# Performance work log

Hardware: AMD Instinct MI355X
Metric: run time of the kernel (lower is better)

The kernel has to match this reference:

```python
import jax, jax.numpy as jnp
import numpy as np

B = 131072
_CNOT_PERM = np.array([0, 1, 3, 2])  # |c t>: 10<->11 swap


def _apply_1q(psi, mats, wire):
    # psi: [B,2,2,2,2] complex, mats: [B,2,2] complex, per-sample single-qubit gate on `wire`
    psi = jnp.moveaxis(psi, wire + 1, -1)
    sh = psi.shape
    psi = psi.reshape(sh[0], -1, 2)
    psi = jnp.einsum('bij,bkj->bki', mats, psi)
    return jnp.moveaxis(psi.reshape(sh), -1, wire + 1)


def _cnot_adj(psi, w):
    # CNOT with control=w, target=w+1 (adjacent wires)
    psi = jnp.moveaxis(psi, (w + 1, w + 2), (-2, -1))
    sh = psi.shape
    psi = psi.reshape(sh[:-2] + (4,))[..., _CNOT_PERM].reshape(sh)
    return jnp.moveaxis(psi, (-2, -1), (w + 1, w + 2))


def _circuit(enc):
    # enc: [B,4] rotation angles; returns [B,4] PauliZ expectations
    b = enc.shape[0]
    half = 0.5 * enc
    c = jnp.cos(half).astype(jnp.complex64)
    s = jnp.sin(half).astype(jnp.complex64)
    z = jnp.zeros_like(c)
    ph = jnp.exp(-1j * half.astype(jnp.complex64))
    ry = jnp.stack([jnp.stack([c, -s], -1), jnp.stack([s, c], -1)], -2)   # [B,4,2,2]
    rz = jnp.stack([jnp.stack([ph, z], -1), jnp.stack([z, jnp.conj(ph)], -1)], -2)
    rx = jnp.stack([jnp.stack([c, -1j * s], -1), jnp.stack([-1j * s, c], -1)], -2)
    psi = jnp.zeros((b, 2, 2, 2, 2), jnp.complex64).at[:, 0, 0, 0, 0].set(1.0)
    for w in range(4):
        psi = _apply_1q(psi, ry[:, w], w)
    for w in range(4):
        psi = _apply_1q(psi, rz[:, w], w)
    for w in range(3):
        psi = _cnot_adj(psi, w)
    for w in range(4):
        psi = _apply_1q(psi, rx[:, w], w)
    probs = psi.real ** 2 + psi.imag ** 2  # [B,2,2,2,2]
    expz = []
    for w in range(4):
        p = jnp.moveaxis(probs, w + 1, 1).reshape(b, 2, -1).sum(-1)
        expz.append(p[:, 0] - p[:, 1])
    return jnp.stack(expz, -1)  # [B,4]


def setup_inputs() -> dict:
    key = jax.random.key(0)
    ks = jax.random.split(key, 9)
    f32 = jnp.float32
    return {
        'x': jax.random.normal(ks[0], (B, 1, 24, 24), f32),
        'W_enc': jax.random.normal(ks[1], (4, 16), f32) * 0.25,
        'b_enc': jax.random.normal(ks[2], (4,), f32) * 0.25,
        'W1': jax.random.normal(ks[3], (32, 4), f32) * 0.5,
        'b1': jax.random.normal(ks[4], (32,), f32) * 0.5,
        'W2': jax.random.normal(ks[5], (4, 32), f32) * 0.17,
        'b2': jax.random.normal(ks[6], (4,), f32) * 0.17,
        'gamma': jnp.ones((4,), f32),
        'beta': jnp.zeros((4,), f32),
    }


def reference(x, W_enc, b_enc, W1, b1, W2, b2, gamma, beta):
    bsz = x.shape[0]
    # avg_pool2d(x, 6): 24x24 -> 4x4, then flatten to 16
    pooled = x.reshape(bsz, 1, 4, 6, 4, 6).mean((3, 5)).reshape(bsz, 16)
    encoded = pooled @ W_enc.T + b_enc            # [B,4]
    out_q = _circuit(encoded)                      # [B,4]
    h = jax.nn.relu(out_q @ W1.T + b1)             # [B,32]
    out = h @ W2.T + b2                            # [B,num_classes]
    # BatchNorm1d in training mode (biased batch variance, eps=1e-5)
    mean = out.mean(0)
    var = ((out - mean) ** 2).mean(0)
    return gamma * (out - mean) / jnp.sqrt(var + 1e-5) + beta
```

## Files before the change

### kernel.cpp

```cpp
#include <hip/hip_runtime.h>

#define BATCH      131072
#define NBLK_MAIN  512
#define NBLK_BN    512

__global__ __launch_bounds__(256, 2) void qnat_main(
    const float* __restrict__ x,
    const float* __restrict__ Wenc, const float* __restrict__ benc,
    const float* __restrict__ W1,   const float* __restrict__ b1,
    const float* __restrict__ W2,   const float* __restrict__ b2,
    float* __restrict__ out_pre, float* __restrict__ partials)
{
    __shared__ float sW[360];
    __shared__ __align__(16) float stage[4][2320];
    __shared__ float pbuf[4][1088];
    __shared__ float redS[4][8];

    const int t = threadIdx.x;
    if (t < 64)  sW[t]       = Wenc[t];
    if (t < 4)   sW[64 + t]  = benc[t];
    if (t < 128) sW[68 + t]  = W1[t];
    if (t < 32)  sW[196 + t] = b1[t];
    if (t < 128) sW[228 + t] = W2[t];
    if (t < 4)   sW[356 + t] = b2[t];
    __syncthreads();

    const int wave = t >> 6, lane = t & 63;
    const int sampleBase = blockIdx.x * 256 + wave * 64;
    float* st = stage[wave];
    float* pb = pbuf[wave];

    const int s_loc = lane >> 4;
    const int slot  = lane & 15;
    const int spr   = slot >> 2, spc = slot & 3;
    const int rdOff = s_loc * 580 + spr * 144 + spc * 6;

    const float4* xg = reinterpret_cast<const float4*>(x);
    const unsigned gbase = (unsigned)sampleBase * 144u;

    float pv[16];
    #pragma unroll
    for (int c = 0; c < 16; ++c) {
        float4 v[9];
        #pragma unroll
        for (int i = 0; i < 9; ++i)
            v[i] = xg[gbase + (unsigned)c * 576u + (unsigned)i * 64u + (unsigned)lane];
        #pragma unroll
        for (int i = 0; i < 9; ++i) {
            const int g = i * 64 + lane;
            const int s = g / 144;
            const int q = g - s * 144;
            *reinterpret_cast<float4*>(&st[s * 580 + q * 4]) = v[i];
        }
        float acc = 0.f;
        #pragma unroll
        for (int r = 0; r < 6; ++r) {
            const float2 a  = *reinterpret_cast<const float2*>(&st[rdOff + r * 24 + 0]);
            const float2 bb = *reinterpret_cast<const float2*>(&st[rdOff + r * 24 + 2]);
            const float2 cc = *reinterpret_cast<const float2*>(&st[rdOff + r * 24 + 4]);
            acc += a.x + a.y + bb.x + bb.y + cc.x + cc.y;
        }
        pv[c] = acc * (1.f / 36.f);
    }

    #pragma unroll
    for (int c = 0; c < 16; ++c)
        pb[(c * 4 + s_loc) * 17 + slot] = pv[c];
    float pooled[16];
    #pragma unroll
    for (int q = 0; q < 16; ++q)
        pooled[q] = pb[lane * 17 + q];

    float ch[4], sh[4];
    #pragma unroll
    for (int j = 0; j < 4; ++j) {
        float e = sW[64 + j];
        #pragma unroll
        for (int k = 0; k < 16; ++k) e = fmaf(pooled[k], sW[j * 16 + k], e);
        const float h = 0.5f * e;
        ch[j] = cosf(h);
        sh[j] = sinf(h);
    }

    float re[16], im[16];
    #pragma unroll
    for (int i = 0; i < 16; ++i) { re[i] = 0.f; im[i] = 0.f; }
    re[0] = 1.f;

    #pragma unroll
    for (int w = 0; w < 4; ++w) {
        const int bit = 8 >> w;
        #pragma unroll
        for (int i = 0; i < 16; ++i) if (!(i & bit)) {
            const int jj = i | bit;
            const float r0 = re[i], m0 = im[i], r1 = re[jj], m1 = im[jj];
            re[i]  = ch[w] * r0 - sh[w] * r1;  im[i]  = ch[w] * m0 - sh[w] * m1;
            re[jj] = sh[w] * r0 + ch[w] * r1;  im[jj] = sh[w] * m0 + ch[w] * m1;
        }
    }
    #pragma unroll
    for (int w = 0; w < 4; ++w) {
        const int bit = 8 >> w;
        #pragma unroll
        for (int i = 0; i < 16; ++i) {
            const float sg = (i & bit) ? 1.f : -1.f;
            const float r = re[i], m = im[i];
            re[i] = ch[w] * r - sg * sh[w] * m;
            im[i] = ch[w] * m + sg * sh[w] * r;
        }
    }
    #define SWAP_AMP(a, b) { float tr = re[a]; re[a] = re[b]; re[b] = tr; \
                             float ti = im[a]; im[a] = im[b]; im[b] = ti; }
    SWAP_AMP(8, 12)  SWAP_AMP(9, 13)  SWAP_AMP(10, 14) SWAP_AMP(11, 15)
    SWAP_AMP(4, 6)   SWAP_AMP(5, 7)   SWAP_AMP(12, 14) SWAP_AMP(13, 15)
    SWAP_AMP(2, 3)   SWAP_AMP(6, 7)   SWAP_AMP(10, 11) SWAP_AMP(14, 15)
    #undef SWAP_AMP

    #pragma unroll
    for (int w = 0; w < 4; ++w) {
        const int bit = 8 >> w;
        #pragma unroll
        for (int i = 0; i < 16; ++i) if (!(i & bit)) {
            const int jj = i | bit;
            const float r0 = re[i], m0 = im[i], r1 = re[jj], m1 = im[jj];
            re[i]  = ch[w] * r0 + sh[w] * m1;  im[i]  = ch[w] * m0 - sh[w] * r1;
            re[jj] = sh[w] * m0 + ch[w] * r1;  im[jj] = ch[w] * m1 - sh[w] * r0;
        }
    }

    float ez[4];
    #pragma unroll
    for (int w = 0; w < 4; ++w) {
        const int bit = 8 >> w;
        float acc = 0.f;
        #pragma unroll
        for (int i = 0; i < 16; ++i) {
            const float p = re[i] * re[i] + im[i] * im[i];
            acc += (i & bit) ? -p : p;
        }
        ez[w] = acc;
    }

    float o0 = sW[356], o1 = sW[357], o2 = sW[358], o3 = sW[359];
    #pragma unroll
    for (int i = 0; i < 32; ++i) {
        float h = sW[196 + i];
        #pragma unroll
        for (int j = 0; j < 4; ++j) h = fmaf(ez[j], sW[68 + i * 4 + j], h);
        h = fmaxf(h, 0.f);
        o0 = fmaf(h, sW[228 +  0 + i], o0);
        o1 = fmaf(h, sW[228 + 32 + i], o1);
        o2 = fmaf(h, sW[228 + 64 + i], o2);
        o3 = fmaf(h, sW[228 + 96 + i], o3);
    }

    reinterpret_cast<float4*>(out_pre)[blockIdx.x * 256 + t] =
        make_float4(o0, o1, o2, o3);

    {
        float v8[8] = { o0, o1, o2, o3, o0 * o0, o1 * o1, o2 * o2, o3 * o3 };
        #pragma unroll
        for (int off = 32; off; off >>= 1) {
            #pragma unroll
            for (int k = 0; k < 8; ++k) v8[k] += __shfl_down(v8[k], off);
        }
        if (lane == 0) {
            #pragma unroll
            for (int k = 0; k < 8; ++k) redS[wave][k] = v8[k];
        }
        __syncthreads();
        if (t < 8) {
            partials[blockIdx.x * 8 + t] =
                redS[0][t] + redS[1][t] + redS[2][t] + redS[3][t];
        }
    }
}

__global__ __launch_bounds__(512) void qnat_reduce(
    const float* __restrict__ partials, const float* __restrict__ gamma,
    const float* __restrict__ beta, float* __restrict__ ss)
{
    const int t = threadIdx.x;
    const float4* p4 = reinterpret_cast<const float4*>(partials);
    const float4 a = p4[t * 2], b = p4[t * 2 + 1];
    float v[8] = { a.x, a.y, a.z, a.w, b.x, b.y, b.z, b.w };
    #pragma unroll
    for (int off = 32; off; off >>= 1) {
        #pragma unroll
        for (int k = 0; k < 8; ++k) v[k] += __shfl_down(v[k], off);
    }
    __shared__ float red[8][8];
    const int wave = t >> 6, lane = t & 63;
    if (lane == 0) {
        #pragma unroll
        for (int k = 0; k < 8; ++k) red[wave][k] = v[k];
    }
    __syncthreads();
    if (t < 4) {
        float sum = 0.f, sumsq = 0.f;
        #pragma unroll
        for (int w = 0; w < 8; ++w) { sum += red[w][t]; sumsq += red[w][4 + t]; }
        const float invB  = 1.f / (float)BATCH;
        const float mean  = sum * invB;
        const float var   = sumsq * invB - mean * mean;
        const float scale = gamma[t] / sqrtf(var + 1e-5f);
        ss[t]     = scale;
        ss[4 + t] = beta[t] - mean * scale;
    }
}

__global__ __launch_bounds__(256) void qnat_bn(
    float* __restrict__ io, const float* __restrict__ ss)
{
    __shared__ float s8[8];
    if (threadIdx.x < 8) s8[threadIdx.x] = ss[threadIdx.x];
    __syncthreads();
    const int idx = blockIdx.x * 256 + threadIdx.x;
    float4* p = reinterpret_cast<float4*>(io);
    float4 v = p[idx];
    v.x = fmaf(v.x, s8[0], s8[4]);
    v.y = fmaf(v.y, s8[1], s8[5]);
    v.z = fmaf(v.z, s8[2], s8[6]);
    v.w = fmaf(v.w, s8[3], s8[7]);
    p[idx] = v;
}

extern "C" void kernel_launch(void* const* d_in, const int* in_sizes, int n_in,
                              void* d_out, int out_size, void* d_ws, size_t ws_size,
                              hipStream_t stream)
{
    const float* x     = (const float*)d_in[0];
    const float* Wenc  = (const float*)d_in[1];
    const float* benc  = (const float*)d_in[2];
    const float* W1    = (const float*)d_in[3];
    const float* b1    = (const float*)d_in[4];
    const float* W2    = (const float*)d_in[5];
    const float* b2    = (const float*)d_in[6];
    const float* gamma = (const float*)d_in[7];
    const float* beta  = (const float*)d_in[8];

    float* out      = (float*)d_out;
    float* partials = (float*)d_ws;
    float* ss       = partials + NBLK_MAIN * 8;

    qnat_main<<<NBLK_MAIN, 256, 0, stream>>>(x, Wenc, benc, W1, b1, W2, b2,
                                             out, partials);
    qnat_reduce<<<1, 512, 0, stream>>>(partials, gamma, beta, ss);
    qnat_bn<<<NBLK_BN, 256, 0, stream>>>(out, ss);
}
```

Baseline: 59.77 us.

## Split each sample across two lanes and double the main-kernel grid

The main kernel now processes 32 samples per wave instead of 64, with two lanes sharing each sample. Each lane computes half of the encoder dot product and the halves are combined with a shuffle. The separate pooling buffer is dropped and the staging buffer reused, which lowers LDS use so the launch bound can ask for 4 blocks per CU. The grid doubles to 1024 blocks and the reduce kernel sums twice as many partials. The cost is that both lanes of a pair run the full quantum-circuit and MLP math redundantly, and the new block-wide __syncthreads calls add barriers.

```diff
diff --git a/kernel.cpp b/kernel.cpp
--- a/kernel.cpp
+++ b/kernel.cpp
@@ -1,10 +1,10 @@
 #include <hip/hip_runtime.h>
 
 #define BATCH      131072
-#define NBLK_MAIN  512
+#define NBLK_MAIN  1024
 #define NBLK_BN    512
 
-__global__ __launch_bounds__(256, 2) void qnat_main(
+__global__ __launch_bounds__(256, 4) void qnat_main(
     const float* __restrict__ x,
     const float* __restrict__ Wenc, const float* __restrict__ benc,
     const float* __restrict__ W1,   const float* __restrict__ b1,
@@ -13,7 +13,6 @@
 {
     __shared__ float sW[360];
     __shared__ __align__(16) float stage[4][2320];
-    __shared__ float pbuf[4][1088];
     __shared__ float redS[4][8];
 
     const int t = threadIdx.x;
@@ -26,9 +25,8 @@
     __syncthreads();
 
     const int wave = t >> 6, lane = t & 63;
-    const int sampleBase = blockIdx.x * 256 + wave * 64;
+    const int waveSampleBase = blockIdx.x * 128 + wave * 32;
     float* st = stage[wave];
-    float* pb = pbuf[wave];
 
     const int s_loc = lane >> 4;
     const int slot  = lane & 15;
@@ -36,11 +34,11 @@
     const int rdOff = s_loc * 580 + spr * 144 + spc * 6;
 
     const float4* xg = reinterpret_cast<const float4*>(x);
-    const unsigned gbase = (unsigned)sampleBase * 144u;
-
-    float pv[16];
-    #pragma unroll
-    for (int c = 0; c < 16; ++c) {
+    const unsigned gbase = (unsigned)waveSampleBase * 144u;
+
+    float pv[8];
+    #pragma unroll
+    for (int c = 0; c < 8; ++c) {
         float4 v[9];
         #pragma unroll
         for (int i = 0; i < 9; ++i)
@@ -63,21 +61,28 @@
         pv[c] = acc * (1.f / 36.f);
     }
 
-    #pragma unroll
-    for (int c = 0; c < 16; ++c)
+    __syncthreads();
+    float* pb = st;
+    #pragma unroll
+    for (int c = 0; c < 8; ++c)
         pb[(c * 4 + s_loc) * 17 + slot] = pv[c];
-    float pooled[16];
-    #pragma unroll
-    for (int q = 0; q < 16; ++q)
-        pooled[q] = pb[lane * 17 + q];
+    __syncthreads();
+
+    const int myS = lane >> 1;
+    const int k0  = (lane & 1) * 8;
+    float p8[8];
+    #pragma unroll
+    for (int q = 0; q < 8; ++q)
+        p8[q] = pb[myS * 17 + k0 + q];
 
     float ch[4], sh[4];
     #pragma unroll
     for (int j = 0; j < 4; ++j) {
-        float e = sW[64 + j];
-        #pragma unroll
-        for (int k = 0; k < 16; ++k) e = fmaf(pooled[k], sW[j * 16 + k], e);
-        const float h = 0.5f * e;
+        float e = 0.f;
+        #pragma unroll
+        for (int q = 0; q < 8; ++q) e = fmaf(p8[q], sW[j * 16 + k0 + q], e);
+        e += __shfl_xor(e, 1);
+        const float h = 0.5f * (e + sW[64 + j]);
         ch[j] = cosf(h);
         sh[j] = sinf(h);
     }
@@ -154,11 +159,14 @@
         o3 = fmaf(h, sW[228 + 96 + i], o3);
     }
 
-    reinterpret_cast<float4*>(out_pre)[blockIdx.x * 256 + t] =
-        make_float4(o0, o1, o2, o3);
+    const int sGlob = waveSampleBase + myS;
+    const float2 ov = (lane & 1) ? make_float2(o2, o3) : make_float2(o0, o1);
+    reinterpret_cast<float2*>(out_pre)[sGlob * 2 + (lane & 1)] = ov;
 
     {
-        float v8[8] = { o0, o1, o2, o3, o0 * o0, o1 * o1, o2 * o2, o3 * o3 };
+        const float m = (lane & 1) ? 0.f : 1.f;
+        float v8[8] = { m * o0, m * o1, m * o2, m * o3,
+                        m * o0 * o0, m * o1 * o1, m * o2 * o2, m * o3 * o3 };
         #pragma unroll
         for (int off = 32; off; off >>= 1) {
             #pragma unroll
@@ -182,8 +190,10 @@
 {
     const int t = threadIdx.x;
     const float4* p4 = reinterpret_cast<const float4*>(partials);
-    const float4 a = p4[t * 2], b = p4[t * 2 + 1];
-    float v[8] = { a.x, a.y, a.z, a.w, b.x, b.y, b.z, b.w };
+    const float4 a0 = p4[t * 4 + 0], a1 = p4[t * 4 + 1];
+    const float4 a2 = p4[t * 4 + 2], a3 = p4[t * 4 + 3];
+    float v[8] = { a0.x + a2.x, a0.y + a2.y, a0.z + a2.z, a0.w + a2.w,
+                   a1.x + a3.x, a1.y + a3.y, a1.z + a3.z, a1.w + a3.w };
     #pragma unroll
     for (int off = 32; off; off >>= 1) {
         #pragma unroll
```

Result: no change. 60.50 us (+1.2%).
